# Optimization experiments

Measured on AMD Instinct MI355X. Metric: run time of the kernel, lower is better.

The kernel has to match this reference:

```python
import jax, jax.numpy as jnp
import numpy as np

B, T, FEATS, HEAD = 2, 2048, 2048, 16
DIM_HEAD = FEATS // HEAD
EPS = float(jnp.finfo(jnp.float32).eps)  # torch nn.RMSNorm default eps=None -> dtype eps


def _rms_norm(u, g):
    # u: [..., d]; torch RMSNorm: u / sqrt(mean(u^2) + eps) * g
    return u * jax.lax.rsqrt(jnp.mean(u * u, axis=-1, keepdims=True) + EPS) * g


def setup_inputs() -> dict:
    key = jax.random.key(0)
    kx, kw = jax.random.split(key)
    x = jax.random.normal(kx, (B, T, FEATS), dtype=jnp.float32)
    W = jax.random.normal(kw, (FEATS, FEATS), dtype=jnp.float32) / np.sqrt(FEATS)
    g1 = jnp.ones((DIM_HEAD,), dtype=jnp.float32)
    g2 = jnp.ones((DIM_HEAD,), dtype=jnp.float32)
    g3 = jnp.ones((DIM_HEAD,), dtype=jnp.float32)
    return {"x": x, "W": W, "g1": g1, "g2": g2, "g3": g3}


def reference(x, W, g1, g2, g3):
    Bb, Tt, C = x.shape
    sqrt_d = jnp.asarray(DIM_HEAD ** 0.5, dtype=x.dtype)
    # tied QKV projection: torch Linear -> x @ W.T ; then split heads -> [B,H,T,D]
    w = (x @ W.T).reshape(Bb, Tt, HEAD, DIM_HEAD).transpose(0, 2, 1, 3)
    q = _rms_norm(w, g1)
    k = _rms_norm(w, g2)
    v = _rms_norm(w, g3)
    att = jnp.einsum("bhid,bhjd->bhij", q, k) / sqrt_d  # [B,H,T,T]
    # symmetric row + column softmax
    score = jax.nn.softmax(att, axis=-1) + jax.nn.softmax(att, axis=-2)
    y = jnp.einsum("bhij,bhjd->bihd", score, v).reshape(Bb, Tt, C)
    # F.linear(y, W.t()) == y @ W  (tied-weight reprojection)
    return y @ W
```

## Files before the change

### kernel.cpp

```cpp
#include <hip/hip_runtime.h>
#include <stdint.h>

#define T_SEQ 2048
#define B_SZ 2
#define N_HEAD 16
#define D_HEAD 128
#define C_DIM 2048
#define M_ROWS (B_SZ*T_SEQ)
#define N_BH (B_SZ*N_HEAD)

typedef _Float16 f16;
typedef f16 f16x8 __attribute__((ext_vector_type(8)));
typedef f16 f16x4 __attribute__((ext_vector_type(4)));
typedef float f32x4 __attribute__((ext_vector_type(4)));

#define MFMA_F16(a,b,c) __builtin_amdgcn_mfma_f32_16x16x32_f16(a,b,c,0,0,0)

#define BAR_LGKM() do { asm volatile("s_waitcnt lgkmcnt(0)" ::: "memory"); \
                        __builtin_amdgcn_s_barrier(); } while (0)
#define BAR_ALL()  do { asm volatile("s_waitcnt vmcnt(0) lgkmcnt(0)" ::: "memory"); \
                        __builtin_amdgcn_s_barrier(); } while (0)

__device__ __forceinline__ void gl_lds16(const void* g, void* l) {
  __builtin_amdgcn_global_load_lds(
      (const __attribute__((address_space(1))) unsigned int*)g,
      (__attribute__((address_space(3))) unsigned int*)l, 16, 0, 0);
}

__global__ void k_prep_w(const float* __restrict__ W, f16* __restrict__ Wb,
                         f16* __restrict__ Wtb) {
  __shared__ float tile[64][65];
  const int bx = blockIdx.x * 64;
  const int by = blockIdx.y * 64;
  const int t = threadIdx.x;
  const int tc = t & 63, tr4 = t >> 6;
  for (int rr = tr4; rr < 64; rr += 4) {
    float v = W[(size_t)(by + rr) * C_DIM + bx + tc];
    tile[rr][tc] = v;
    Wb[(size_t)(by + rr) * C_DIM + bx + tc] = (f16)v;
  }
  __syncthreads();
  for (int rr = tr4; rr < 64; rr += 4) {
    Wtb[(size_t)(bx + rr) * C_DIM + by + tc] = (f16)tile[tc][rr];
  }
}

__global__ void k_prep_x(const float* __restrict__ x, f16* __restrict__ xb) {
  int i = blockIdx.x * blockDim.x + threadIdx.x;
  const int stride = gridDim.x * blockDim.x;
  const int n4 = (M_ROWS * C_DIM) / 4;
  for (; i < n4; i += stride) {
    f32x4 v = ((const f32x4*)x)[i];
    f16x4 o; o[0]=(f16)v[0]; o[1]=(f16)v[1]; o[2]=(f16)v[2]; o[3]=(f16)v[3];
    ((f16x4*)xb)[i] = o;
  }
}

template<typename OT>
__global__ __launch_bounds__(256, 2)
void k_gemm_bt(const f16* __restrict__ A, const f16* __restrict__ Bm,
               OT* __restrict__ C, int Nd, int Kd) {
  __shared__ __align__(16) f16 As[2][128 * 64];
  __shared__ __align__(16) f16 Bs[2][128 * 64];
  const int tid = threadIdx.x;
  const int lane = tid & 63, wid = tid >> 6;
  const int lr = lane & 15, lkg = lane >> 4;
  const int wr = wid >> 1, wc = wid & 1;
  const int tm = blockIdx.y * 128, tn = blockIdx.x * 128;

  f32x4 acc[4][4];
#pragma unroll
  for (int i = 0; i < 4; ++i)
#pragma unroll
    for (int j = 0; j < 4; ++j) acc[i][j] = (f32x4){0.f, 0.f, 0.f, 0.f};

  const int nkt = Kd >> 6;

  auto stage = [&](int buf, int kt) {
    const int k0 = kt << 6;
    for (int s = 0; s < 4; ++s) {
      const int r0 = (wid * 4 + s) * 8;
      const int r = r0 + (lane >> 3);
      const int lg = ((lane & 7) ^ (r & 7)) << 3;
      gl_lds16(A + (size_t)(tm + r) * Kd + k0 + lg, &As[buf][r0 * 64]);
      gl_lds16(Bm + (size_t)(tn + r) * Kd + k0 + lg, &Bs[buf][r0 * 64]);
    }
  };

  stage(0, 0);
  int cur = 0;
  for (int kt = 0; kt < nkt; ++kt) {
    __syncthreads();
    if (kt + 1 < nkt) stage(cur ^ 1, kt + 1);
#pragma unroll
    for (int kk = 0; kk < 2; ++kk) {
      f16x8 a[4], b[4];
#pragma unroll
      for (int i = 0; i < 4; ++i) {
        const int ra = wr * 64 + i * 16 + lr;
        const int ga = ((kk * 4 + lkg) ^ (ra & 7)) << 3;
        a[i] = *(const f16x8*)&As[cur][ra * 64 + ga];
        const int rb = wc * 64 + i * 16 + lr;
        const int gb = ((kk * 4 + lkg) ^ (rb & 7)) << 3;
        b[i] = *(const f16x8*)&Bs[cur][rb * 64 + gb];
      }
#pragma unroll
      for (int i = 0; i < 4; ++i)
#pragma unroll
        for (int j = 0; j < 4; ++j) acc[i][j] = MFMA_F16(a[i], b[j], acc[i][j]);
    }
    cur ^= 1;
  }
#pragma unroll
  for (int i = 0; i < 4; ++i) {
    const int row0 = tm + wr * 64 + i * 16 + lkg * 4;
#pragma unroll
    for (int j = 0; j < 4; ++j) {
      const int col = tn + wc * 64 + j * 16 + lr;
#pragma unroll
      for (int r = 0; r < 4; ++r)
        C[(size_t)(row0 + r) * Nd + col] = (OT)acc[i][j][r];
    }
  }
}

__global__ __launch_bounds__(256, 4)
void k_rms(const f16* __restrict__ wb, const float* __restrict__ g1,
           const float* __restrict__ g2, f16* __restrict__ nb,
           f16* __restrict__ mb) {
  const int tid = threadIdx.x, lane = tid & 63, wid = tid >> 6;
  const int lr = lane & 15, grp = lane >> 4;
  float gs[8];
#pragma unroll
  for (int e = 0; e < 8; ++e)
    gs[e] = g1[lr * 8 + e] * g2[lr * 8 + e] * 0.08838834764831843f;
  const int R = blockIdx.x * 16 + wid * 4 + grp;
  const f16x8 w8 = *(const f16x8*)&wb[(size_t)R * 128 + lr * 8];
  float f[8];
  float ss = 0.f;
#pragma unroll
  for (int e = 0; e < 8; ++e) { f[e] = (float)w8[e]; ss += f[e] * f[e]; }
  ss += __shfl_xor(ss, 1); ss += __shfl_xor(ss, 2);
  ss += __shfl_xor(ss, 4); ss += __shfl_xor(ss, 8);
  const float scale = rsqrtf(ss * (1.f / 128.f) + 1.1920928955078125e-07f);
  const int hh = R & (N_HEAD - 1);
  const int bt = R >> 4;
  const int b = bt >> 11;
  const int t = bt & (T_SEQ - 1);
  const size_t dst = ((size_t)((b * N_HEAD + hh) * T_SEQ + t)) * 128 + lr * 8;
  f16x8 n8, m8;
#pragma unroll
  for (int e = 0; e < 8; ++e) {
    float nf = f[e] * scale;
    n8[e] = (f16)nf;
    m8[e] = (f16)(nf * gs[e]);
  }
  *(f16x8*)&nb[dst] = n8;
  *(f16x8*)&mb[dst] = m8;
}

__global__ void k_tn(const f16* __restrict__ nin, f16* __restrict__ nT) {
  __shared__ __align__(16) f16 tile[64][72];
  const int t = threadIdx.x;
  const int c = t & 7, r4 = t >> 3;
  const int bh = blockIdx.z, t0 = blockIdx.x * 64, d0 = blockIdx.y * 64;
  const f16* src = nin + ((size_t)bh * T_SEQ + t0) * 128 + d0;
  for (int rr = r4; rr < 64; rr += 32)
    *(f16x8*)&tile[rr][c * 8] = *(const f16x8*)&src[(size_t)rr * 128 + c * 8];
  __syncthreads();
  f16* dst = nT + ((size_t)bh * 128 + d0) * T_SEQ + t0;
  for (int rr = r4; rr < 64; rr += 32) {
    f16x8 v;
#pragma unroll
    for (int e = 0; e < 8; ++e) v[e] = tile[c * 8 + e][rr];
    *(f16x8*)&dst[(size_t)rr * T_SEQ + c * 8] = v;
  }
}

__global__ __launch_bounds__(256, 2)
void k_stats(const f16* __restrict__ mIn, const f16* __restrict__ nIn,
             float* __restrict__ alpha) {
  __shared__ __align__(16) f16 Ms[128 * 128];
  __shared__ __align__(16) f16 Ns[128 * 128];
  __shared__ float red[256];
  const int tid = threadIdx.x, lane = tid & 63, wid = tid >> 6;
  const int lr = lane & 15, lkg = lane >> 4;
  const int wr = wid >> 1, wc = wid & 1;
  const int it = blockIdx.x, bh = blockIdx.y;
  const f16* mp = mIn + (size_t)bh * T_SEQ * 128;
  const f16* np = nIn + (size_t)bh * T_SEQ * 128;

  auto stageM = [&]() {
    for (int s = 0; s < 8; ++s) {
      const int r0 = (wid * 8 + s) * 4;
      const int r = r0 + (lane >> 4);
      const int lg = ((lane & 15) ^ (r & 7)) << 3;
      gl_lds16(mp + (size_t)(it * 128 + r) * 128 + lg, &Ms[r0 * 128]);
    }
  };
  auto stageN = [&](int jt) {
    for (int s = 0; s < 8; ++s) {
      const int r0 = (wid * 8 + s) * 4;
      const int r = r0 + (lane >> 4);
      const int lg = ((lane & 15) ^ (r & 7)) << 3;
      gl_lds16(np + (size_t)(jt * 128 + r) * 128 + lg, &Ns[r0 * 128]);
    }
  };

  float srun[16];
#pragma unroll
  for (int q = 0; q < 16; ++q) srun[q] = 0.f;

  stageM();
  stageN(0);
  __syncthreads();
  for (int jt = 0; jt < 16; ++jt) {
    f32x4 acc[4][4];
#pragma unroll
    for (int i = 0; i < 4; ++i)
#pragma unroll
      for (int j = 0; j < 4; ++j) acc[i][j] = (f32x4){0.f, 0.f, 0.f, 0.f};
#pragma unroll
    for (int kk = 0; kk < 4; ++kk) {
      f16x8 a[4], b[4];
#pragma unroll
      for (int i = 0; i < 4; ++i) {
        const int ra = wr * 64 + i * 16 + lr;
        const int ga = ((kk * 4 + lkg) ^ (ra & 7)) << 3;
        a[i] = *(const f16x8*)&Ms[ra * 128 + ga];
        const int rb = wc * 64 + i * 16 + lr;
        const int gb = ((kk * 4 + lkg) ^ (rb & 7)) << 3;
        b[i] = *(const f16x8*)&Ns[rb * 128 + gb];
      }
#pragma unroll
      for (int i = 0; i < 4; ++i)
#pragma unroll
        for (int j = 0; j < 4; ++j) acc[i][j] = MFMA_F16(a[i], b[j], acc[i][j]);
    }
    __syncthreads();
    if (jt < 15) stageN(jt + 1);
#pragma unroll
    for (int i = 0; i < 4; ++i)
#pragma unroll
      for (int r = 0; r < 4; ++r) {
        float s = __expf(acc[i][0][r]) + __expf(acc[i][1][r]) +
                  __expf(acc[i][2][r]) + __expf(acc[i][3][r]);
        srun[i * 4 + r] += s;
      }
    __syncthreads();
  }
#pragma unroll
  for (int q = 0; q < 16; ++q) {
    float v = srun[q];
    v += __shfl_xor(v, 1); v += __shfl_xor(v, 2);
    v += __shfl_xor(v, 4); v += __shfl_xor(v, 8);
    srun[q] = v;
  }
  if (lr == 0) {
#pragma unroll
    for (int q = 0; q < 16; ++q) {
      const int row = wr * 64 + (q >> 2) * 16 + lkg * 4 + (q & 3);
      red[row * 2 + wc] = srun[q];
    }
  }
  __syncthreads();
  if (tid < 128) {
    const float s = red[tid * 2] + red[tid * 2 + 1];
    alpha[(size_t)bh * T_SEQ + it * 128 + tid] = 1.f / s;
  }
}

__global__ __launch_bounds__(256, 2)
void k_apply(const f16* __restrict__ mIn, const f16* __restrict__ nIn,
             const f16* __restrict__ nTIn, const float* __restrict__ alpha,
             const float* __restrict__ g3, f16* __restrict__ yb) {
  __shared__ __align__(16) f16 Ms[128 * 128];
  __shared__ __align__(16) f16 Ns[64 * 128];
  __shared__ __align__(16) f16 Nts[128 * 64];
  __shared__ __align__(16) f16 Ps[128 * 64];
  const int tid = threadIdx.x, lane = tid & 63, wid = tid >> 6;
  const int lr = lane & 15, lkg = lane >> 4;
  const int wj = wid >> 1;
  const int wi = wid & 1;
  const int it = blockIdx.x, bh = blockIdx.y;
  const int b = bh >> 4, hh = bh & 15;
  const f16* mp = mIn + (size_t)bh * T_SEQ * 128;
  const f16* np = nIn + (size_t)bh * T_SEQ * 128;
  const f16* ntp = nTIn + (size_t)bh * 128 * T_SEQ;
  const float* al = alpha + (size_t)bh * T_SEQ;

  auto stageM = [&]() {
#pragma unroll
    for (int s = 0; s < 8; ++s) {
      const int r0 = (wid * 8 + s) * 4;
      const int r = r0 + (lane >> 4);
      const int lg = ((lane & 15) ^ (r & 7)) << 3;
      gl_lds16(mp + (size_t)(it * 128 + r) * 128 + lg, &Ms[r0 * 128]);
    }
  };
  auto stageN = [&](int jt) {
#pragma unroll
    for (int s = 0; s < 4; ++s) {
      const int r0 = (wid * 4 + s) * 4;
      const int r = r0 + (lane >> 4);
      const int lg = ((lane & 15) ^ (r & 7)) << 3;
      gl_lds16(np + (size_t)(jt * 64 + r) * 128 + lg, &Ns[r0 * 128]);
    }
  };
  f16x8 ntreg[4];
  auto ldNT = [&](int jt) {
    const int d = tid >> 1;
    const f16* src = ntp + (size_t)d * T_SEQ + jt * 64 + (tid & 1) * 32;
#pragma unroll
    for (int c = 0; c < 4; ++c) ntreg[c] = *(const f16x8*)(src + c * 8);
  };
  auto wrNT = [&]() {
    const int d = tid >> 1;
#pragma unroll
    for (int c = 0; c < 4; ++c) {
      const int gj = (tid & 1) * 4 + c;
      *(f16x8*)&Nts[d * 64 + ((gj ^ (d & 7)) << 3)] = ntreg[c];
    }
  };

  float ai[4], g3v[16];
#pragma unroll
  for (int ii = 0; ii < 4; ++ii) ai[ii] = al[it * 128 + wi * 64 + ii * 16 + lr];
#pragma unroll
  for (int dd = 0; dd < 4; ++dd)
#pragma unroll
    for (int r = 0; r < 4; ++r)
      g3v[dd * 4 + r] = g3[wj * 64 + dd * 16 + lkg * 4 + r];

  f32x4 yacc[4][4];
#pragma unroll
  for (int i = 0; i < 4; ++i)
#pragma unroll
    for (int j = 0; j < 4; ++j) yacc[i][j] = (f32x4){0.f, 0.f, 0.f, 0.f};

  stageM();
  stageN(0);
  ldNT(0);
  wrNT();
  BAR_ALL();

  for (int jt = 0; jt < 32; ++jt) {
    if (jt < 31) ldNT(jt + 1);
    float aj[8];
#pragma unroll
    for (int jj = 0; jj < 2; ++jj)
#pragma unroll
      for (int r = 0; r < 4; ++r)
        aj[jj * 4 + r] = al[jt * 64 + wj * 32 + jj * 16 + lkg * 4 + r];

    f32x4 acc[2][4];
#pragma unroll
    for (int i = 0; i < 2; ++i)
#pragma unroll
      for (int j = 0; j < 4; ++j) acc[i][j] = (f32x4){0.f, 0.f, 0.f, 0.f};
#pragma unroll
    for (int kk = 0; kk < 4; ++kk) {
      f16x8 a[2], bfr[4];
#pragma unroll
      for (int jj = 0; jj < 2; ++jj) {
        const int jrow = wj * 32 + jj * 16 + lr;
        a[jj] = *(const f16x8*)&Ns[jrow * 128 + (((kk * 4 + lkg) ^ (jrow & 7)) << 3)];
      }
#pragma unroll
      for (int ii = 0; ii < 4; ++ii) {
        const int irow = wi * 64 + ii * 16 + lr;
        bfr[ii] = *(const f16x8*)&Ms[irow * 128 + (((kk * 4 + lkg) ^ (irow & 7)) << 3)];
      }
#pragma unroll
      for (int jj = 0; jj < 2; ++jj)
#pragma unroll
        for (int ii = 0; ii < 4; ++ii)
          acc[jj][ii] = MFMA_F16(a[jj], bfr[ii], acc[jj][ii]);
    }
    BAR_LGKM();
    if (jt < 31) stageN(jt + 1);

#pragma unroll
    for (int jj = 0; jj < 2; ++jj)
#pragma unroll
      for (int ii = 0; ii < 4; ++ii) {
        f16x4 o;
#pragma unroll
        for (int r = 0; r < 4; ++r) {
          const float p = __expf(acc[jj][ii][r]) * (ai[ii] + aj[jj * 4 + r]);
          o[r] = (f16)p;
        }
        const int il = wi * 64 + ii * 16 + lr;
        const int jl = wj * 32 + jj * 16 + lkg * 4;
        *(f16x4*)&Ps[il * 64 + (((jl >> 3) ^ (il & 7)) << 3) + (jl & 7)] = o;
      }
    BAR_LGKM();

#pragma unroll
    for (int kk = 0; kk < 2; ++kk) {
      f16x8 a[4], bfr[4];
#pragma unroll
      for (int dd = 0; dd < 4; ++dd) {
        const int drow = wj * 64 + dd * 16 + lr;
        a[dd] = *(const f16x8*)&Nts[drow * 64 + (((kk * 4 + lkg) ^ (drow & 7)) << 3)];
      }
#pragma unroll
      for (int ii = 0; ii < 4; ++ii) {
        const int irow = wi * 64 + ii * 16 + lr;
        bfr[ii] = *(const f16x8*)&Ps[irow * 64 + (((kk * 4 + lkg) ^ (irow & 7)) << 3)];
      }
#pragma unroll
      for (int dd = 0; dd < 4; ++dd)
#pragma unroll
        for (int ii = 0; ii < 4; ++ii)
          yacc[dd][ii] = MFMA_F16(a[dd], bfr[ii], yacc[dd][ii]);
    }
    BAR_LGKM();
    if (jt < 31) wrNT();
    BAR_ALL();
  }

#pragma unroll
  for (int dd = 0; dd < 4; ++dd) {
    const int d0 = wj * 64 + dd * 16 + lkg * 4;
#pragma unroll
    for (int ii = 0; ii < 4; ++ii) {
      const int icol = wi * 64 + ii * 16 + lr;
      const size_t base =
          ((size_t)(b * T_SEQ + it * 128 + icol)) * C_DIM + hh * 128 + d0;
      f16x4 o;
#pragma unroll
      for (int r = 0; r < 4; ++r) o[r] = (f16)(yacc[dd][ii][r] * g3v[dd * 4 + r]);
      *(f16x4*)&yb[base] = o;
    }
  }
}

extern "C" void kernel_launch(void* const* d_in, const int* in_sizes, int n_in,
                              void* d_out, int out_size, void* d_ws,
                              size_t ws_size, hipStream_t stream) {
  const float* x = (const float*)d_in[0];
  const float* W = (const float*)d_in[1];
  const float* g1 = (const float*)d_in[2];
  const float* g2 = (const float*)d_in[3];
  const float* g3 = (const float*)d_in[4];
  float* out = (float*)d_out;
  char* ws = (char*)d_ws;

  f16* xb   = (f16*)(ws);
  f16* Wb   = (f16*)(ws + 16777216);
  f16* Wtb  = (f16*)(ws + 25165824);
  f16* wb   = (f16*)(ws + 33554432);
  f16* nb   = (f16*)(ws + 50331648);
  f16* mb   = (f16*)(ws + 67108864);
  f16* nT   = (f16*)(ws + 83886080);
  f16* yb   = (f16*)(ws + 100663296);
  float* alpha = (float*)(ws + 117440512);

  k_prep_w<<<dim3(32, 32), 256, 0, stream>>>(W, Wb, Wtb);
  k_prep_x<<<dim3(2048), 256, 0, stream>>>(x, xb);
  k_gemm_bt<f16><<<dim3(16, 32), 256, 0, stream>>>(xb, Wb, wb, C_DIM, C_DIM);
  k_rms<<<dim3(4096), 256, 0, stream>>>(wb, g1, g2, nb, mb);
  k_tn<<<dim3(32, 2, 32), 256, 0, stream>>>(nb, nT);
  k_stats<<<dim3(16, 32), 256, 0, stream>>>(mb, nb, alpha);
  k_apply<<<dim3(16, 32), 256, 0, stream>>>(mb, nb, nT, alpha, g3, yb);
  k_gemm_bt<float><<<dim3(16, 32), 256, 0, stream>>>(yb, Wtb, out, C_DIM, C_DIM);
}
```

Baseline: 246.7 us.

## Keep M tile in registers and double-buffer N tiles in stats/apply kernels

In both attention kernels the query-side M tile is now loaded once into per-wave registers instead of shared memory. N tiles are double-buffered in LDS so the next tile's async load overlaps the current compute, with one barrier per iteration. In k_apply the transposed N operand is loaded straight from global into MFMA-fragment registers, removing the Nts LDS buffer and its write pass. This cuts LDS traffic and barriers but raises register pressure (msr plus ntreg), which under launch_bounds(256,2) risks spills or lower occupancy. The next transposed-N load is issued late, after the second MFMA loop, so its latency may not be fully hidden.

```diff
diff --git a/kernel.cpp b/kernel.cpp
--- a/kernel.cpp
+++ b/kernel.cpp
@@ -180,8 +180,7 @@
 __global__ __launch_bounds__(256, 2)
 void k_stats(const f16* __restrict__ mIn, const f16* __restrict__ nIn,
              float* __restrict__ alpha) {
-  __shared__ __align__(16) f16 Ms[128 * 128];
-  __shared__ __align__(16) f16 Ns[128 * 128];
+  __shared__ __align__(16) f16 Ns[2][128 * 128];
   __shared__ float red[256];
   const int tid = threadIdx.x, lane = tid & 63, wid = tid >> 6;
   const int lr = lane & 15, lkg = lane >> 4;
@@ -190,31 +189,33 @@
   const f16* mp = mIn + (size_t)bh * T_SEQ * 128;
   const f16* np = nIn + (size_t)bh * T_SEQ * 128;
 
-  auto stageM = [&]() {
+  f16x8 msr[4][4];
+#pragma unroll
+  for (int i = 0; i < 4; ++i)
+#pragma unroll
+    for (int kk = 0; kk < 4; ++kk)
+      msr[i][kk] = *(const f16x8*)&mp[(size_t)(it * 128 + wr * 64 + i * 16 + lr) * 128 +
+                                      (kk * 4 + lkg) * 8];
+
+  auto stageN = [&](int buf, int jt) {
+#pragma unroll
     for (int s = 0; s < 8; ++s) {
       const int r0 = (wid * 8 + s) * 4;
       const int r = r0 + (lane >> 4);
       const int lg = ((lane & 15) ^ (r & 7)) << 3;
-      gl_lds16(mp + (size_t)(it * 128 + r) * 128 + lg, &Ms[r0 * 128]);
+      gl_lds16(np + (size_t)(jt * 128 + r) * 128 + lg, &Ns[buf][r0 * 128]);
     }
   };
-  auto stageN = [&](int jt) {
-    for (int s = 0; s < 8; ++s) {
-      const int r0 = (wid * 8 + s) * 4;
-      const int r = r0 + (lane >> 4);
-      const int lg = ((lane & 15) ^ (r & 7)) << 3;
-      gl_lds16(np + (size_t)(jt * 128 + r) * 128 + lg, &Ns[r0 * 128]);
-    }
-  };
 
   float srun[16];
 #pragma unroll
   for (int q = 0; q < 16; ++q) srun[q] = 0.f;
 
-  stageM();
-  stageN(0);
-  __syncthreads();
+  stageN(0, 0);
+  BAR_ALL();
+  int cur = 0;
   for (int jt = 0; jt < 16; ++jt) {
+    if (jt < 15) stageN(cur ^ 1, jt + 1);
     f32x4 acc[4][4];
 #pragma unroll
     for (int i = 0; i < 4; ++i)
@@ -222,23 +223,19 @@
       for (int j = 0; j < 4; ++j) acc[i][j] = (f32x4){0.f, 0.f, 0.f, 0.f};
 #pragma unroll
     for (int kk = 0; kk < 4; ++kk) {
-      f16x8 a[4], b[4];
-#pragma unroll
-      for (int i = 0; i < 4; ++i) {
-        const int ra = wr * 64 + i * 16 + lr;
-        const int ga = ((kk * 4 + lkg) ^ (ra & 7)) << 3;
-        a[i] = *(const f16x8*)&Ms[ra * 128 + ga];
-        const int rb = wc * 64 + i * 16 + lr;
+      f16x8 b[4];
+#pragma unroll
+      for (int j = 0; j < 4; ++j) {
+        const int rb = wc * 64 + j * 16 + lr;
         const int gb = ((kk * 4 + lkg) ^ (rb & 7)) << 3;
-        b[i] = *(const f16x8*)&Ns[rb * 128 + gb];
+        b[j] = *(const f16x8*)&Ns[cur][rb * 128 + gb];
       }
 #pragma unroll
       for (int i = 0; i < 4; ++i)
 #pragma unroll
-        for (int j = 0; j < 4; ++j) acc[i][j] = MFMA_F16(a[i], b[j], acc[i][j]);
-    }
-    __syncthreads();
-    if (jt < 15) stageN(jt + 1);
+        for (int j = 0; j < 4; ++j)
+          acc[i][j] = MFMA_F16(msr[i][kk], b[j], acc[i][j]);
+    }
 #pragma unroll
     for (int i = 0; i < 4; ++i)
 #pragma unroll
@@ -247,7 +244,8 @@
                   __expf(acc[i][2][r]) + __expf(acc[i][3][r]);
         srun[i * 4 + r] += s;
       }
-    __syncthreads();
+    BAR_ALL();
+    cur ^= 1;
   }
 #pragma unroll
   for (int q = 0; q < 16; ++q) {
@@ -274,9 +272,7 @@
 void k_apply(const f16* __restrict__ mIn, const f16* __restrict__ nIn,
              const f16* __restrict__ nTIn, const float* __restrict__ alpha,
              const float* __restrict__ g3, f16* __restrict__ yb) {
-  __shared__ __align__(16) f16 Ms[128 * 128];
-  __shared__ __align__(16) f16 Ns[64 * 128];
-  __shared__ __align__(16) f16 Nts[128 * 64];
+  __shared__ __align__(16) f16 Ns[2][64 * 128];
   __shared__ __align__(16) f16 Ps[128 * 64];
   const int tid = threadIdx.x, lane = tid & 63, wid = tid >> 6;
   const int lr = lane & 15, lkg = lane >> 4;
@@ -289,48 +285,36 @@
   const f16* ntp = nTIn + (size_t)bh * 128 * T_SEQ;
   const float* al = alpha + (size_t)bh * T_SEQ;
 
-  auto stageM = [&]() {
-#pragma unroll
-    for (int s = 0; s < 8; ++s) {
-      const int r0 = (wid * 8 + s) * 4;
-      const int r = r0 + (lane >> 4);
-      const int lg = ((lane & 15) ^ (r & 7)) << 3;
-      gl_lds16(mp + (size_t)(it * 128 + r) * 128 + lg, &Ms[r0 * 128]);
-    }
-  };
-  auto stageN = [&](int jt) {
+  f16x8 msr[4][4];
+#pragma unroll
+  for (int ii = 0; ii < 4; ++ii)
+#pragma unroll
+    for (int kk = 0; kk < 4; ++kk)
+      msr[ii][kk] = *(const f16x8*)&mp[(size_t)(it * 128 + wi * 64 + ii * 16 + lr) * 128 +
+                                       (kk * 4 + lkg) * 8];
+
+  auto stageN = [&](int buf, int jt) {
 #pragma unroll
     for (int s = 0; s < 4; ++s) {
       const int r0 = (wid * 4 + s) * 4;
       const int r = r0 + (lane >> 4);
       const int lg = ((lane & 15) ^ (r & 7)) << 3;
-      gl_lds16(np + (size_t)(jt * 64 + r) * 128 + lg, &Ns[r0 * 128]);
+      gl_lds16(np + (size_t)(jt * 64 + r) * 128 + lg, &Ns[buf][r0 * 128]);
     }
   };
-  f16x8 ntreg[4];
+  f16x8 ntreg[4][2];
   auto ldNT = [&](int jt) {
-    const int d = tid >> 1;
-    const f16* src = ntp + (size_t)d * T_SEQ + jt * 64 + (tid & 1) * 32;
-#pragma unroll
-    for (int c = 0; c < 4; ++c) ntreg[c] = *(const f16x8*)(src + c * 8);
+#pragma unroll
+    for (int dd = 0; dd < 4; ++dd)
+#pragma unroll
+      for (int kk = 0; kk < 2; ++kk)
+        ntreg[dd][kk] = *(const f16x8*)&ntp[(size_t)(wj * 64 + dd * 16 + lr) * T_SEQ +
+                                            jt * 64 + (kk * 4 + lkg) * 8];
   };
-  auto wrNT = [&]() {
-    const int d = tid >> 1;
-#pragma unroll
-    for (int c = 0; c < 4; ++c) {
-      const int gj = (tid & 1) * 4 + c;
-      *(f16x8*)&Nts[d * 64 + ((gj ^ (d & 7)) << 3)] = ntreg[c];
-    }
-  };
-
-  float ai[4], g3v[16];
+
+  float ai[4];
 #pragma unroll
   for (int ii = 0; ii < 4; ++ii) ai[ii] = al[it * 128 + wi * 64 + ii * 16 + lr];
-#pragma unroll
-  for (int dd = 0; dd < 4; ++dd)
-#pragma unroll
-    for (int r = 0; r < 4; ++r)
-      g3v[dd * 4 + r] = g3[wj * 64 + dd * 16 + lkg * 4 + r];
 
   f32x4 yacc[4][4];
 #pragma unroll
@@ -338,14 +322,12 @@
 #pragma unroll
     for (int j = 0; j < 4; ++j) yacc[i][j] = (f32x4){0.f, 0.f, 0.f, 0.f};
 
-  stageM();
-  stageN(0);
+  stageN(0, 0);
   ldNT(0);
-  wrNT();
   BAR_ALL();
-
+  int cur = 0;
   for (int jt = 0; jt < 32; ++jt) {
-    if (jt < 31) ldNT(jt + 1);
+    if (jt < 31) stageN(cur ^ 1, jt + 1);
     float aj[8];
 #pragma unroll
     for (int jj = 0; jj < 2; ++jj)
@@ -360,25 +342,18 @@
       for (int j = 0; j < 4; ++j) acc[i][j] = (f32x4){0.f, 0.f, 0.f, 0.f};
 #pragma unroll
     for (int kk = 0; kk < 4; ++kk) {
-      f16x8 a[2], bfr[4];
+      f16x8 a[2];
 #pragma unroll
       for (int jj = 0; jj < 2; ++jj) {
         const int jrow = wj * 32 + jj * 16 + lr;
-        a[jj] = *(const f16x8*)&Ns[jrow * 128 + (((kk * 4 + lkg) ^ (jrow & 7)) << 3)];
-      }
-#pragma unroll
-      for (int ii = 0; ii < 4; ++ii) {
-        const int irow = wi * 64 + ii * 16 + lr;
-        bfr[ii] = *(const f16x8*)&Ms[irow * 128 + (((kk * 4 + lkg) ^ (irow & 7)) << 3)];
+        a[jj] = *(const f16x8*)&Ns[cur][jrow * 128 + (((kk * 4 + lkg) ^ (jrow & 7)) << 3)];
       }
 #pragma unroll
       for (int jj = 0; jj < 2; ++jj)
 #pragma unroll
         for (int ii = 0; ii < 4; ++ii)
-          acc[jj][ii] = MFMA_F16(a[jj], bfr[ii], acc[jj][ii]);
-    }
-    BAR_LGKM();
-    if (jt < 31) stageN(jt + 1);
+          acc[jj][ii] = MFMA_F16(a[jj], msr[ii][kk], acc[jj][ii]);
+    }
 
 #pragma unroll
     for (int jj = 0; jj < 2; ++jj)
@@ -398,12 +373,7 @@
 
 #pragma unroll
     for (int kk = 0; kk < 2; ++kk) {
-      f16x8 a[4], bfr[4];
-#pragma unroll
-      for (int dd = 0; dd < 4; ++dd) {
-        const int drow = wj * 64 + dd * 16 + lr;
-        a[dd] = *(const f16x8*)&Nts[drow * 64 + (((kk * 4 + lkg) ^ (drow & 7)) << 3)];
-      }
+      f16x8 bfr[4];
 #pragma unroll
       for (int ii = 0; ii < 4; ++ii) {
         const int irow = wi * 64 + ii * 16 + lr;
@@ -413,16 +383,19 @@
       for (int dd = 0; dd < 4; ++dd)
 #pragma unroll
         for (int ii = 0; ii < 4; ++ii)
-          yacc[dd][ii] = MFMA_F16(a[dd], bfr[ii], yacc[dd][ii]);
-    }
-    BAR_LGKM();
-    if (jt < 31) wrNT();
+          yacc[dd][ii] = MFMA_F16(ntreg[dd][kk], bfr[ii], yacc[dd][ii]);
+    }
+    if (jt < 31) ldNT(jt + 1);
     BAR_ALL();
+    cur ^= 1;
   }
 
 #pragma unroll
   for (int dd = 0; dd < 4; ++dd) {
     const int d0 = wj * 64 + dd * 16 + lkg * 4;
+    float g3v[4];
+#pragma unroll
+    for (int r = 0; r < 4; ++r) g3v[r] = g3[d0 + r];
 #pragma unroll
     for (int ii = 0; ii < 4; ++ii) {
       const int icol = wi * 64 + ii * 16 + lr;
@@ -430,7 +403,7 @@
           ((size_t)(b * T_SEQ + it * 128 + icol)) * C_DIM + hh * 128 + d0;
       f16x4 o;
 #pragma unroll
-      for (int r = 0; r < 4; ++r) o[r] = (f16)(yacc[dd][ii][r] * g3v[dd * 4 + r]);
+      for (int r = 0; r < 4; ++r) o[r] = (f16)(yacc[dd][ii][r] * g3v[r]);
       *(f16x4*)&yb[base] = o;
     }
   }
```

New measurement: 289.8 us. 1.17x slower.
